# Optimization experiments

Hardware: AMD Instinct MI355X
Metric: run time of the kernel (lower is better)

The kernel has to match this reference:

```python
import jax, jax.numpy as jnp
import numpy as np

B, N, RD = 32, 2000, 32
E, H, A = 128, 256, 8
NUM_ACTIONS = N
ACTION_NORM = float(NUM_ACTIONS)


def _mlp2(x, W1, b1, W2, b2):
    return jnp.maximum(x @ W1 + b1, 0.0) @ W2 + b2


def setup_inputs() -> dict:
    key = jax.random.key(0)
    ks = jax.random.split(key, 8)
    s = lambda fan_in: 1.0 / np.sqrt(fan_in)
    return {
        "state": jax.random.normal(ks[0], (B, N, RD), jnp.float32),
        "distance_matrix": jax.random.uniform(ks[1], (N, N), jnp.float32),
        "W_emb1": jax.random.normal(ks[2], (RD, H), jnp.float32) * s(RD),
        "b_emb1": jnp.zeros((H,), jnp.float32),
        "W_emb2": jax.random.normal(ks[3], (H, E), jnp.float32) * s(H),
        "b_emb2": jnp.zeros((E,), jnp.float32),
        "Wq1": jax.random.normal(ks[4], (E + A, H), jnp.float32) * s(E + A),
        "bq1": jnp.zeros((H,), jnp.float32),
        "Wq2": jax.random.normal(ks[5], (H, 1), jnp.float32) * s(H),
        "bq2": jnp.zeros((1,), jnp.float32),
        "fixed_actions": jax.random.randint(ks[6], (3, B), 0, NUM_ACTIONS, jnp.int32),
        "fixed_agent_ids": jnp.arange(3, dtype=jnp.int32),
    }


def reference(state, distance_matrix, W_emb1, b_emb1, W_emb2, b_emb2,
              Wq1, bq1, Wq2, bq2, fixed_actions, fixed_agent_ids):
    # normalized distance -> similarity, row-stochastic
    dm = distance_matrix / distance_matrix.max()
    sim = jnp.exp(-dm)  # scaling = 1 (use_nn_scaling=False)
    sim = sim / sim.sum(-1, keepdims=True)

    enc = _mlp2(state, W_emb1, b_emb1, W_emb2, b_emb2)      # [B,N,E]
    x = jnp.einsum('nm,bme->bne', sim, enc)                 # graph conv mix

    idx_f = jnp.arange(N, dtype=x.dtype)

    def qnet(actions):
        # actions: [B,A] broadcast over node axis -> concat -> MLP -> [B,N]
        act = jnp.broadcast_to(actions[:, None, :], (B, N, A))
        feat = jnp.concatenate([x, act], axis=-1)           # [B,N,E+A]
        return _mlp2(feat, Wq1, bq1, Wq2, bq2)[..., 0]      # [B,N]

    # init actions: -1 everywhere, fixed agents get given action / norm
    actions = jnp.full((B, A), -1.0, dtype=x.dtype)
    actions = actions.at[:, fixed_agent_ids].set(
        fixed_actions.T.astype(x.dtype) / ACTION_NORM)

    # sequential per-agent soft-argmax loop (second torch loop; the first
    # torch loop's q-values are fully overwritten here, so it is dead code)
    q_cols = []
    for agent_id in range(A):
        q = qnet(actions)                                   # [B,N]
        sam = jnp.clip(jax.nn.softmax(q, axis=-1) @ idx_f, 0.0, float(NUM_ACTIONS))
        actions = actions.at[:, agent_id].set(
            jax.lax.stop_gradient(sam / ACTION_NORM))
        q2 = qnet(actions)
        qv = jnp.take_along_axis(q2, sam.astype(jnp.int32)[:, None], axis=-1)[:, 0]
        q_cols.append(qv)

    q_values = jnp.stack(q_cols, axis=1)                    # [B,A]
    chosen = (actions * ACTION_NORM).astype(jnp.int32)      # [B,A]
    return q_values, chosen
```

## Files before the change

### kernel.cpp

```cpp
#include <hip/hip_runtime.h>
#include <cstddef>

#define NB 32
#define NN 2000
#define NRD 32
#define NE 128
#define NH 256
#define NA 8
#define KP8 2048
#define NGP 128
#define H1S 264
#define XT8S 136
#define ACTION_NORM 2000.0f

typedef unsigned short u16;
typedef unsigned char u8;
typedef __bf16 b16x8 __attribute__((ext_vector_type(8)));
typedef float f32x4 __attribute__((ext_vector_type(4)));
typedef const __attribute__((address_space(1))) unsigned int* gptr_t;
typedef __attribute__((address_space(3))) unsigned int* lptr_t;

__device__ inline u16 f2bf(float x) {
    unsigned u = __float_as_uint(x);
    u += 0x7FFFu + ((u >> 16) & 1u);
    return (u16)(u >> 16);
}
__device__ inline float bf2f(u16 h) { return __uint_as_float((unsigned)h << 16); }
__device__ inline u8 f2fp8(float x) {
    return (u8)(__builtin_amdgcn_cvt_pk_fp8_f32(x, x, 0, false) & 0xFF);
}
__device__ inline u16 f2fp8x2(float a, float b) {
    return (u16)(__builtin_amdgcn_cvt_pk_fp8_f32(a, b, 0, false) & 0xFFFF);
}
__device__ inline float fp82f(u8 b) {
    return __builtin_amdgcn_cvt_pk_f32_fp8((unsigned)b, false)[0];
}
__device__ inline int kswz(int m) {
    return (m & ~63) + (((m >> 3) & 3) << 4) + (((m >> 5) & 1) << 3) + (m & 7);
}

#define PREP_STATE (64000 * 32)
#define PREP_W1T   (256 * 32)
#define PREP_W2T   (128 * 256)
#define PREP_WQ1T  (256 * 128)
#define PREP_PAD   (4096 * 48)
#define PREP_TOT   (PREP_STATE + PREP_W1T + PREP_W2T + PREP_WQ1T + PREP_PAD)
#define PREP_BLOCKS (PREP_TOT / 256)
#define MAX_BLOCKS 1024
__global__ __launch_bounds__(256) void k_front(
        const float* __restrict__ state, const float* __restrict__ W1,
        const float* __restrict__ W2, const float* __restrict__ Wq1,
        const float* __restrict__ dm, const int* __restrict__ fa,
        const int* __restrict__ fid,
        u16* __restrict__ state_b, u16* __restrict__ W1t,
        u16* __restrict__ W2t, u8* __restrict__ Wq1f8,
        u8* __restrict__ encb, float* __restrict__ pmax,
        float* __restrict__ actions, float* __restrict__ ap0,
        float2* __restrict__ part0) {
    __shared__ float sh[256];
    const int blk = blockIdx.x, t = threadIdx.x;
    if (blk < PREP_BLOCKS) {
        int i = blk * 256 + t;
        if (i < PREP_STATE) { state_b[i] = f2bf(state[i]); return; }
        i -= PREP_STATE;
        if (i < PREP_W1T) { int h = i >> 5, k = i & 31; W1t[i] = f2bf(W1[k * NH + h]); return; }
        i -= PREP_W1T;
        if (i < PREP_W2T) { int e = i >> 8, h = i & 255; W2t[i] = f2bf(W2[h * NE + e]); return; }
        i -= PREP_W2T;
        if (i < PREP_WQ1T) { int hq = i >> 7, e = i & 127; Wq1f8[i] = f2fp8(Wq1[e * NH + hq]); return; }
        i -= PREP_WQ1T;
        if (i < PREP_PAD) { int eb = i / 48, mm = NN + (i % 48); encb[(size_t)eb * KP8 + kswz(mm)] = 0; }
        return;
    }
    if (blk < PREP_BLOCKS + MAX_BLOCKS) {
        const int bid = blk - PREP_BLOCKS;
        float m = 0.0f;
        for (size_t i = (size_t)bid * 256 + t; i < (size_t)NN * NN; i += (size_t)MAX_BLOCKS * 256)
            m = fmaxf(m, dm[i]);
        sh[t] = m; __syncthreads();
        for (int s = 128; s > 0; s >>= 1) {
            if (t < s) sh[t] = fmaxf(sh[t], sh[t + s]);
            __syncthreads();
        }
        if (t == 0) pmax[bid] = sh[0];
        return;
    }
    const int b = t >> 3, a = t & 7;
    float v = -1.0f;
    for (int j = 0; j < 3; ++j)
        if (fid[j] == a) v = (float)fa[j * NB + b] / ACTION_NORM;
    actions[t] = v;
    sh[t] = v;
    __syncthreads();
    float wq[NA];
#pragma unroll
    for (int aa = 0; aa < NA; ++aa) wq[aa] = Wq1[(size_t)(NE + aa) * NH + t];
    for (int bb = 0; bb < NB; ++bb) {
        float s = 0.0f;
#pragma unroll
        for (int aa = 0; aa < NA; ++aa) s = fmaf(sh[bb * NA + aa], wq[aa], s);
        ap0[bb * NH + t] = s;
    }
    for (int i = t; i < NB * NGP; i += 256) part0[i] = make_float2(0.0f, 0.0f);
}

__global__ __launch_bounds__(512) void k_sim_enc(
        const u16* __restrict__ state_b, const u16* __restrict__ W1t,
        const u16* __restrict__ W2t, u8* __restrict__ encb,
        const float* __restrict__ b1, const float* __restrict__ b2,
        const float* __restrict__ dm, const float* __restrict__ pmax,
        u8* __restrict__ simb, float* __restrict__ inv_rs) {
    __shared__ u16 stage[20 * 512];
    __shared__ u16 h1t[64 * H1S];
    const int blk = blockIdx.x, tid = threadIdx.x;

    if (blk >= 1000) {
        float* shf = (float*)stage;
        const int n = blk - 1000, t = tid;
        float m = fmaxf(pmax[t], pmax[t + 512]);
        shf[t] = m; __syncthreads();
        for (int s = 256; s > 0; s >>= 1) {
            if (t < s) shf[t] = fmaxf(shf[t], shf[t + s]);
            __syncthreads();
        }
        const float inv = 1.0f / shf[0];
        __syncthreads();
        float s = 0.0f;
        for (int mm = t * 2; mm < KP8; mm += 1024) {
            float e0 = 0.0f, e1 = 0.0f;
            if (mm < NN)     { e0 = expf(-dm[(size_t)n * NN + mm] * inv);     s += e0; }
            if (mm + 1 < NN) { e1 = expf(-dm[(size_t)n * NN + mm + 1] * inv); s += e1; }
            *(u16*)(simb + (size_t)n * KP8 + kswz(mm)) = f2fp8x2(e0, e1);
        }
        shf[t] = s; __syncthreads();
        for (int st = 256; st > 0; st >>= 1) {
            if (t < st) shf[t] += shf[t + st];
            __syncthreads();
        }
        if (t == 0) inv_rs[n] = 1.0f / shf[0];
        return;
    }

    const int w = tid >> 6, l = tid & 63;
    const int lm = l & 15, lq = l >> 4;
    const int gm = blk * 64;

    {
#pragma unroll
        for (int i = 0; i < 3; ++i) {
            const int idx = w * 3 + i;
            if (idx < 20) {
                const u16* gp;
                if (idx < 4) gp = state_b + (size_t)(gm + idx * 16 + lm) * NRD + lq * 8;
                else         gp = W1t + (size_t)((idx - 4) * 16 + lm) * NRD + lq * 8;
                __builtin_amdgcn_global_load_lds((gptr_t)gp, (lptr_t)(stage + idx * 512), 16, 0, 0);
            }
        }
        __syncthreads();
        b16x8 af[4], bf[2];
#pragma unroll
        for (int i = 0; i < 4; ++i) af[i] = *(const b16x8*)(stage + i * 512 + l * 8);
#pragma unroll
        for (int j = 0; j < 2; ++j) bf[j] = *(const b16x8*)(stage + (4 + w * 2 + j) * 512 + l * 8);
        f32x4 acc1[4][2] = {};
#pragma unroll
        for (int i = 0; i < 4; ++i)
#pragma unroll
            for (int j = 0; j < 2; ++j)
                acc1[i][j] = __builtin_amdgcn_mfma_f32_16x16x32_bf16(af[i], bf[j], acc1[i][j], 0, 0, 0);
#pragma unroll
        for (int i = 0; i < 4; ++i)
#pragma unroll
            for (int r = 0; r < 4; ++r) {
                const int row = i * 16 + lq * 4 + r;
#pragma unroll
                for (int j = 0; j < 2; ++j) {
                    const int col = w * 32 + j * 16 + lm;
                    h1t[row * H1S + col] = f2bf(fmaxf(acc1[i][j][r] + b1[col], 0.0f));
                }
            }
    }

    const int wr = w & 3, wc = w >> 2;
    f32x4 acc2[2][2] = {};
    const u16* gpw = W2t + (size_t)(w * 16 + lm) * NH + lq * 8;
    __syncthreads();
    __builtin_amdgcn_global_load_lds((gptr_t)gpw, (lptr_t)(stage + w * 512), 16, 0, 0);
    __syncthreads();
    for (int t = 0; t < 8; ++t) {
        const int cur = t & 1;
        if (t < 7) {
            gpw += 32;
            __builtin_amdgcn_global_load_lds((gptr_t)gpw,
                (lptr_t)(stage + (cur ^ 1) * 4096 + w * 512), 16, 0, 0);
        }
        const u16* base = stage + cur * 4096;
        b16x8 af2[2], bf2[2];
#pragma unroll
        for (int i = 0; i < 2; ++i)
            af2[i] = *(const b16x8*)(base + (wr * 2 + i) * 512 + l * 8);
#pragma unroll
        for (int j = 0; j < 2; ++j)
            bf2[j] = *(const b16x8*)(h1t + (wc * 32 + j * 16 + lm) * H1S + t * 32 + lq * 8);
#pragma unroll
        for (int i = 0; i < 2; ++i)
#pragma unroll
            for (int j = 0; j < 2; ++j)
                acc2[i][j] = __builtin_amdgcn_mfma_f32_16x16x32_bf16(af2[i], bf2[j], acc2[i][j], 0, 0, 0);
        __syncthreads();
    }

    u8* etile = (u8*)stage;
#pragma unroll
    for (int i = 0; i < 2; ++i)
#pragma unroll
        for (int r = 0; r < 4; ++r) {
            const int e = wr * 32 + i * 16 + lq * 4 + r;
            const float bias = b2[e];
#pragma unroll
            for (int j = 0; j < 2; ++j) {
                const int off = wc * 32 + j * 16 + lm;
                etile[e * 64 + off] = f2fp8(acc2[i][j][r] + bias);
            }
        }
    __syncthreads();
#pragma unroll
    for (int u0 = 0; u0 < 2; ++u0) {
        const int u = u0 * 512 + tid;
        const int e = u >> 3, run = u & 7;
        const int rg0 = gm + run * 8;
        const unsigned bb = (unsigned)rg0 / 2000u;
        const unsigned m0 = (unsigned)rg0 - bb * 2000u;
        const int wbyte = (int)(m0 & ~63u) + (int)(((m0 >> 3) & 3u) << 4) + (int)(((m0 >> 5) & 1u) << 3);
        const uint2 v = *(const uint2*)(etile + e * 64 + run * 8);
        *(uint2*)(encb + ((size_t)bb * 128 + e) * KP8 + wbyte) = v;
    }
}

__global__ __launch_bounds__(512) void k_conv_y0(
        const u8* __restrict__ simb, const u8* __restrict__ encb,
        const u8* __restrict__ Wq1f8, const float* __restrict__ inv_rs,
        const float* __restrict__ bq1, const float* __restrict__ ap0,
        const float* __restrict__ Wq2, u8* __restrict__ y0f8,
        float2* __restrict__ part0) {
    __shared__ u8 lds[4 * 16384];
    __shared__ float qsum[64 * 8];
    const int tid = threadIdx.x;
    const int w = tid >> 6, l = tid & 63;
    const int wr = w & 1, wc = w >> 1;
    const int bm = blockIdx.x * 128;
    const int bb = blockIdx.y;
    const int lm = l & 15, lq = l >> 4;
    const u8* Bt = encb + (size_t)bb * 128 * KP8;
    typedef long lx2 __attribute__((ext_vector_type(2)));

    f32x4 acc[4][2] = {};

    const u8* gpt[2];
#pragma unroll
    for (int i = 0; i < 2; ++i) {
        const int idx = w * 2 + i;
        if (idx < 8) {
            int row = bm + idx * 16 + lm;
            row = row < NN ? row : NN - 1;
            gpt[i] = simb + (size_t)row * KP8 + lq * 16;
        } else {
            gpt[i] = Bt + (size_t)((idx - 8) * 16 + lm) * KP8 + lq * 16;
        }
    }

    auto STAGE = [&](int kt, int buf) {
#pragma unroll
        for (int i = 0; i < 2; ++i)
            __builtin_amdgcn_global_load_lds((gptr_t)(gpt[i] + kt * 64),
                (lptr_t)(lds + buf * 16384 + (w * 2 + i) * 1024), 16, 0, 0);
    };
    auto COMPUTE = [&](int buf) {
        const u8* curb = lds + buf * 16384;
        const int fo = l * 16;
        lx2 af[4], bf[2];
#pragma unroll
        for (int i = 0; i < 4; ++i)
            af[i] = *(const lx2*)(curb + (wr * 4 + i) * 1024 + fo);
#pragma unroll
        for (int j = 0; j < 2; ++j)
            bf[j] = *(const lx2*)(curb + (8 + wc * 2 + j) * 1024 + fo);
        __builtin_amdgcn_s_setprio(1);
#pragma unroll
        for (int i = 0; i < 4; ++i)
#pragma unroll
            for (int j = 0; j < 2; ++j) {
                acc[i][j] = __builtin_amdgcn_mfma_f32_16x16x32_fp8_fp8(af[i][0], bf[j][0], acc[i][j], 0, 0, 0);
                acc[i][j] = __builtin_amdgcn_mfma_f32_16x16x32_fp8_fp8(af[i][1], bf[j][1], acc[i][j], 0, 0, 0);
            }
        __builtin_amdgcn_s_setprio(0);
    };

#define FENCE() __builtin_amdgcn_sched_barrier(0)
#define BAR_VM(N) do { FENCE(); asm volatile("s_waitcnt vmcnt(" #N ")" ::: "memory"); \
    __builtin_amdgcn_s_barrier(); FENCE(); } while (0)

    STAGE(0, 0);
    STAGE(1, 1);
    for (int t = 0; t < 30; ++t) {
        STAGE(t + 2, (t + 2) & 3);
        BAR_VM(4);
        COMPUTE(t & 3);
    }
    BAR_VM(2);
    COMPUTE(2);
    BAR_VM(0);
    COMPUTE(3);
#undef BAR_VM
#undef FENCE

#pragma unroll
    for (int i = 0; i < 4; ++i) {
#pragma unroll
        for (int r = 0; r < 4; ++r) {
            const int row = wr * 64 + i * 16 + lq * 4 + r;
            const int gn = bm + row;
            const float rsv = inv_rs[gn < NN ? gn : NN - 1];
#pragma unroll
            for (int j = 0; j < 2; ++j) {
                const int col = wc * 32 + j * 16 + lm;
                lds[row * XT8S + col] = f2fp8(acc[i][j][r] * rsv);
            }
        }
    }
    __syncthreads();

    const int h0 = w * 32;
    float bq1v[2], apv[2], w2vv[2];
#pragma unroll
    for (int j = 0; j < 2; ++j) {
        const int h = h0 + j * 16 + lm;
        bq1v[j] = bq1[h];
        apv[j] = ap0[bb * NH + h];
        w2vv[j] = Wq2[h];
    }
    float se_tot = 0.0f, sn_tot = 0.0f;

    for (int half = 0; half < 2; ++half) {
        f32x4 acc2[4][2] = {};
#pragma unroll
        for (int ks = 0; ks < 4; ++ks) {
            long bfw[2];
#pragma unroll
            for (int j = 0; j < 2; ++j)
                bfw[j] = *(const long*)(Wq1f8 + (size_t)(h0 + j * 16 + lm) * NE + ks * 32 + lq * 8);
#pragma unroll
            for (int i = 0; i < 4; ++i) {
                const long afx = *(const long*)(lds + (half * 64 + i * 16 + lm) * XT8S + ks * 32 + lq * 8);
#pragma unroll
                for (int j = 0; j < 2; ++j)
                    acc2[i][j] = __builtin_amdgcn_mfma_f32_16x16x32_fp8_fp8(afx, bfw[j], acc2[i][j], 0, 0, 0);
            }
        }
#pragma unroll
        for (int i = 0; i < 4; ++i) {
#pragma unroll
            for (int r = 0; r < 4; ++r) {
                const int rl = i * 16 + lq * 4 + r;
                const int n = bm + half * 64 + rl;
                float q = 0.0f;
#pragma unroll
                for (int j = 0; j < 2; ++j) {
                    const float v = acc2[i][j][r] + bq1v[j];
                    if (n < NN) y0f8[((size_t)n * NB + bb) * NH + h0 + j * 16 + lm] = f2fp8(v);
                    q += fmaxf(v + apv[j], 0.0f) * w2vv[j];
                }
#pragma unroll
                for (int off = 1; off < 16; off <<= 1) q += __shfl_xor(q, off);
                if (lm == 0) qsum[rl * 8 + w] = q;
            }
        }
        __syncthreads();
        if (tid < 64) {
            const int n = bm + half * 64 + tid;
            float q = 0.0f;
#pragma unroll
            for (int wv = 0; wv < 8; ++wv) q += qsum[tid * 8 + wv];
            float e = (n < NN) ? expf(fminf(q, 60.0f)) : 0.0f;
            float sne = e * (float)n;
#pragma unroll
            for (int off = 32; off > 0; off >>= 1) {
                e += __shfl_xor(e, off); sne += __shfl_xor(sne, off);
            }
            if (tid == 0) { se_tot += e; sn_tot += sne; }
        }
        __syncthreads();
    }
    if (tid == 0) part0[bb * NGP + blockIdx.x] = make_float2(se_tot, sn_tot);
}

__global__ __launch_bounds__(256) void k_agent(
        const u8* __restrict__ y0f8, const float* __restrict__ Wq1,
        const float* __restrict__ Wq2, const float* __restrict__ bq2,
        float* actions, const float2* __restrict__ pin, float2* __restrict__ pout,
        float* __restrict__ out, int ag) {
    __shared__ float sh[256];
    __shared__ float s_sam;
    const int t = threadIdx.x;
    const int lane = t & 63, wave = t >> 6;
    const int wg = blockIdx.x * 4 + wave;
    const int b = wg & 31, ng = wg >> 5;
    const int hl = lane & 15, qtr = lane >> 4;

    float act[NA];
#pragma unroll
    for (int a = 0; a < NA; ++a) act[a] = actions[b * NA + a];
    {
        const float2 p0 = pin[b * NGP + lane];
        const float2 p1 = pin[b * NGP + 64 + lane];
        float se0 = p0.x + p1.x, sn0 = p0.y + p1.y;
#pragma unroll
        for (int m = 32; m > 0; m >>= 1) {
            se0 += __shfl_xor(se0, m); sn0 += __shfl_xor(sn0, m);
        }
        const float sam = fminf(fmaxf(sn0 / se0, 0.0f), 2000.0f);
        act[ag - 1] = sam * (1.0f / ACTION_NORM);
    }
    float ap16[16] = {};
#pragma unroll
    for (int a = 0; a < NA; ++a) {
        const float av = act[a];
        const float4* wq = (const float4*)(Wq1 + (size_t)(NE + a) * NH + hl * 16);
#pragma unroll
        for (int jj = 0; jj < 4; ++jj) {
            const float4 w4 = wq[jj];
            ap16[jj * 4 + 0] = fmaf(av, w4.x, ap16[jj * 4 + 0]);
            ap16[jj * 4 + 1] = fmaf(av, w4.y, ap16[jj * 4 + 1]);
            ap16[jj * 4 + 2] = fmaf(av, w4.z, ap16[jj * 4 + 2]);
            ap16[jj * 4 + 3] = fmaf(av, w4.w, ap16[jj * 4 + 3]);
        }
    }
    float w2v[16];
    {
        const float4* w2p = (const float4*)(Wq2 + hl * 16);
#pragma unroll
        for (int jj = 0; jj < 4; ++jj) {
            const float4 w4 = w2p[jj];
            w2v[jj * 4 + 0] = w4.x; w2v[jj * 4 + 1] = w4.y;
            w2v[jj * 4 + 2] = w4.z; w2v[jj * 4 + 3] = w4.w;
        }
    }

    float se = 0.0f, sn = 0.0f;
#pragma unroll
    for (int k = 0; k < 4; ++k) {
        const int p = ng + k * NGP;
        if (p >= NN / 4) break;
        const int n = 4 * p + qtr;
        const uint4 yv = *(const uint4*)(y0f8 + (((size_t)n * NB + b) << 8) + hl * 16);
        const unsigned dw[4] = {yv.x, yv.y, yv.z, yv.w};
        float q = 0.0f;
#pragma unroll
        for (int d = 0; d < 4; ++d) {
            const auto lo = __builtin_amdgcn_cvt_pk_f32_fp8(dw[d], false);
            const auto hi = __builtin_amdgcn_cvt_pk_f32_fp8(dw[d], true);
            q += fmaxf(lo[0] + ap16[d * 4 + 0], 0.f) * w2v[d * 4 + 0];
            q += fmaxf(lo[1] + ap16[d * 4 + 1], 0.f) * w2v[d * 4 + 1];
            q += fmaxf(hi[0] + ap16[d * 4 + 2], 0.f) * w2v[d * 4 + 2];
            q += fmaxf(hi[1] + ap16[d * 4 + 3], 0.f) * w2v[d * 4 + 3];
        }
#pragma unroll
        for (int off = 1; off < 16; off <<= 1) q += __shfl_xor(q, off);
        const float e = expf(fminf(q, 60.0f));
        se += e; sn += e * (float)n;
    }
    se += __shfl_xor(se, 16); sn += __shfl_xor(sn, 16);
    se += __shfl_xor(se, 32); sn += __shfl_xor(sn, 32);
    if (lane == 0) pout[b * NGP + ng] = make_float2(se, sn);

    if (blockIdx.x < NB) {
        const int bb = blockIdx.x;
        if (wave == 0) {
            const float2 p0 = pin[bb * NGP + lane];
            const float2 p1 = pin[bb * NGP + 64 + lane];
            float a1 = p0.x + p1.x, a2 = p0.y + p1.y;
#pragma unroll
            for (int m = 32; m > 0; m >>= 1) {
                a1 += __shfl_xor(a1, m); a2 += __shfl_xor(a2, m);
            }
            if (lane == 0) s_sam = fminf(fmaxf(a2 / a1, 0.0f), 2000.0f);
        }
        __syncthreads();
        const float sam = s_sam;
        const float samn = sam * (1.0f / ACTION_NORM);
        float apt = 0.0f;
#pragma unroll
        for (int a = 0; a < NA; ++a) {
            const float av = (a == ag - 1) ? samn : actions[bb * NA + a];
            apt = fmaf(av, Wq1[(size_t)(NE + a) * NH + t], apt);
        }
        int nsel = (int)sam; if (nsel > NN - 1) nsel = NN - 1;
        const float yv = fp82f(y0f8[((size_t)nsel * NB + bb) * NH + t]);
        sh[t] = fmaxf(yv + apt, 0.0f) * Wq2[t];
        __syncthreads();
        for (int s = 128; s > 0; s >>= 1) {
            if (t < s) sh[t] += sh[t + s];
            __syncthreads();
        }
        if (t == 0) {
            out[bb * NA + (ag - 1)] = sh[0] + bq2[0];
            actions[bb * NA + (ag - 1)] = samn;
        }
    }
}

__global__ __launch_bounds__(256) void k_fin(
        const u8* __restrict__ y0f8, const float* __restrict__ Wq1,
        const float* __restrict__ Wq2, const float* __restrict__ bq2,
        const float* __restrict__ actions, const float2* __restrict__ pin,
        float* __restrict__ out) {
    __shared__ float sh[256];
    __shared__ float s_sam;
    const int bb = blockIdx.x, t = threadIdx.x;
    const int lane = t & 63, wave = t >> 6;
    if (wave == 0) {
        const float2 p0 = pin[bb * NGP + lane];
        const float2 p1 = pin[bb * NGP + 64 + lane];
        float a1 = p0.x + p1.x, a2 = p0.y + p1.y;
#pragma unroll
        for (int m = 32; m > 0; m >>= 1) {
            a1 += __shfl_xor(a1, m); a2 += __shfl_xor(a2, m);
        }
        if (lane == 0) s_sam = fminf(fmaxf(a2 / a1, 0.0f), 2000.0f);
    }
    __syncthreads();
    const float sam = s_sam;
    const float samn = sam * (1.0f / ACTION_NORM);
    float apt = 0.0f;
#pragma unroll
    for (int a = 0; a < NA; ++a) {
        const float av = (a == NA - 1) ? samn : actions[bb * NA + a];
        apt = fmaf(av, Wq1[(size_t)(NE + a) * NH + t], apt);
    }
    int nsel = (int)sam; if (nsel > NN - 1) nsel = NN - 1;
    const float yv = fp82f(y0f8[((size_t)nsel * NB + bb) * NH + t]);
    sh[t] = fmaxf(yv + apt, 0.0f) * Wq2[t];
    __syncthreads();
    for (int s = 128; s > 0; s >>= 1) {
        if (t < s) sh[t] += sh[t + s];
        __syncthreads();
    }
    if (t == 0) out[bb * NA + (NA - 1)] = sh[0] + bq2[0];
    if (t < NA) {
        const float av = (t == NA - 1) ? samn : actions[bb * NA + t];
        out[NB * NA + bb * NA + t] = (float)(int)(av * ACTION_NORM);
    }
}

extern "C" void kernel_launch(void* const* d_in, const int* in_sizes, int n_in,
                              void* d_out, int out_size, void* d_ws, size_t ws_size,
                              hipStream_t stream) {
    const float* state = (const float*)d_in[0];
    const float* dm    = (const float*)d_in[1];
    const float* W1    = (const float*)d_in[2];
    const float* b1    = (const float*)d_in[3];
    const float* W2    = (const float*)d_in[4];
    const float* b2    = (const float*)d_in[5];
    const float* Wq1   = (const float*)d_in[6];
    const float* bq1   = (const float*)d_in[7];
    const float* Wq2   = (const float*)d_in[8];
    const float* bq2   = (const float*)d_in[9];
    const int* fa      = (const int*)d_in[10];
    const int* fid     = (const int*)d_in[11];
    float* out = (float*)d_out;

    char* p = (char*)d_ws;
    u8* simb       = (u8*)p;       p += (size_t)NN * KP8;
    u8* encb       = (u8*)p;       p += (size_t)4096 * KP8;
    float* inv_rs  = (float*)p;    p += 2048 * 4;
    float* pmax    = (float*)p;    p += 1024 * 4;
    float* actions = (float*)p;    p += 256 * 4;
    float* ap0     = (float*)p;    p += 8192 * 4;
    float2* part0  = (float2*)p;   p += (size_t)NB * NGP * 8;
    float2* part1  = (float2*)p;   p += (size_t)NB * NGP * 8;
    u16* state_b   = (u16*)p;      p += (size_t)2048000 * 2;
    u16* W1t       = (u16*)p;      p += 8192 * 2;
    u16* W2t       = (u16*)p;      p += 32768 * 2;
    u8* Wq1f8      = (u8*)p;       p += 32768;
    u8* y0f8       = (u8*)p;       p += (size_t)16384000;

    k_front<<<PREP_BLOCKS + MAX_BLOCKS + 1, 256, 0, stream>>>(
        state, W1, W2, Wq1, dm, fa, fid,
        state_b, W1t, W2t, Wq1f8, encb, pmax, actions, ap0, part0);
    k_sim_enc<<<3000, 512, 0, stream>>>(state_b, W1t, W2t, encb, b1, b2,
                                        dm, pmax, simb, inv_rs);
    k_conv_y0<<<dim3(16, 32), 512, 0, stream>>>(simb, encb, Wq1f8, inv_rs, bq1,
                                                ap0, Wq2, y0f8, part0);
    for (int ag = 1; ag < NA; ++ag) {
        const float2* pin  = (ag & 1) ? part0 : part1;
        float2*       pout = (ag & 1) ? part1 : part0;
        k_agent<<<1024, 256, 0, stream>>>(y0f8, Wq1, Wq2, bq2, actions,
                                          pin, pout, out, ag);
    }
    k_fin<<<NB, 256, 0, stream>>>(y0f8, Wq1, Wq2, bq2, actions, part1, out);
}
```

Before: 256.8 us.

## Split sim/enc kernels, incremental action projection, and hoisted y0 loads in agent

```diff
diff --git a/kernel.cpp b/kernel.cpp
--- a/kernel.cpp
+++ b/kernel.cpp
@@ -104,43 +104,43 @@
     for (int i = t; i < NB * NGP; i += 256) part0[i] = make_float2(0.0f, 0.0f);
 }
 
-__global__ __launch_bounds__(512) void k_sim_enc(
+__global__ __launch_bounds__(512) void k_sim(
+        const float* __restrict__ dm, const float* __restrict__ pmax,
+        u8* __restrict__ simb, float* __restrict__ inv_rs) {
+    __shared__ float shf[512];
+    __shared__ u8 srow[KP8];
+    const int n = blockIdx.x, t = threadIdx.x;
+    float m = fmaxf(pmax[t], pmax[t + 512]);
+    shf[t] = m; __syncthreads();
+    for (int s = 256; s > 0; s >>= 1) {
+        if (t < s) shf[t] = fmaxf(shf[t], shf[t + s]);
+        __syncthreads();
+    }
+    const float inv = 1.0f / shf[0];
+    __syncthreads();
+    float s = 0.0f;
+    for (int mm = t * 2; mm < KP8; mm += 1024) {
+        float e0 = 0.0f, e1 = 0.0f;
+        if (mm < NN)     { e0 = expf(-dm[(size_t)n * NN + mm] * inv);     s += e0; }
+        if (mm + 1 < NN) { e1 = expf(-dm[(size_t)n * NN + mm + 1] * inv); s += e1; }
+        *(u16*)(srow + kswz(mm)) = f2fp8x2(e0, e1);
+    }
+    shf[t] = s; __syncthreads();
+    for (int st = 256; st > 0; st >>= 1) {
+        if (t < st) shf[t] += shf[t + st];
+        __syncthreads();
+    }
+    if (t == 0) inv_rs[n] = 1.0f / shf[0];
+    if (t < 128) *(uint4*)(simb + (size_t)n * KP8 + t * 16) = *(const uint4*)(srow + t * 16);
+}
+
+__global__ __launch_bounds__(512) void k_enc(
         const u16* __restrict__ state_b, const u16* __restrict__ W1t,
         const u16* __restrict__ W2t, u8* __restrict__ encb,
-        const float* __restrict__ b1, const float* __restrict__ b2,
-        const float* __restrict__ dm, const float* __restrict__ pmax,
-        u8* __restrict__ simb, float* __restrict__ inv_rs) {
+        const float* __restrict__ b1, const float* __restrict__ b2) {
     __shared__ u16 stage[20 * 512];
     __shared__ u16 h1t[64 * H1S];
     const int blk = blockIdx.x, tid = threadIdx.x;
-
-    if (blk >= 1000) {
-        float* shf = (float*)stage;
-        const int n = blk - 1000, t = tid;
-        float m = fmaxf(pmax[t], pmax[t + 512]);
-        shf[t] = m; __syncthreads();
-        for (int s = 256; s > 0; s >>= 1) {
-            if (t < s) shf[t] = fmaxf(shf[t], shf[t + s]);
-            __syncthreads();
-        }
-        const float inv = 1.0f / shf[0];
-        __syncthreads();
-        float s = 0.0f;
-        for (int mm = t * 2; mm < KP8; mm += 1024) {
-            float e0 = 0.0f, e1 = 0.0f;
-            if (mm < NN)     { e0 = expf(-dm[(size_t)n * NN + mm] * inv);     s += e0; }
-            if (mm + 1 < NN) { e1 = expf(-dm[(size_t)n * NN + mm + 1] * inv); s += e1; }
-            *(u16*)(simb + (size_t)n * KP8 + kswz(mm)) = f2fp8x2(e0, e1);
-        }
-        shf[t] = s; __syncthreads();
-        for (int st = 256; st > 0; st >>= 1) {
-            if (t < st) shf[t] += shf[t + st];
-            __syncthreads();
-        }
-        if (t == 0) inv_rs[n] = 1.0f / shf[0];
-        return;
-    }
-
     const int w = tid >> 6, l = tid & 63;
     const int lm = l & 15, lq = l >> 4;
     const int gm = blk * 64;
@@ -397,7 +397,9 @@
 __global__ __launch_bounds__(256) void k_agent(
         const u8* __restrict__ y0f8, const float* __restrict__ Wq1,
         const float* __restrict__ Wq2, const float* __restrict__ bq2,
-        float* actions, const float2* __restrict__ pin, float2* __restrict__ pout,
+        float* actions, const int* __restrict__ fa, const int* __restrict__ fid,
+        const float* __restrict__ apb, float* __restrict__ apbase_out,
+        const float2* __restrict__ pin, float2* __restrict__ pout,
         float* __restrict__ out, int ag) {
     __shared__ float sh[256];
     __shared__ float s_sam;
@@ -406,10 +408,9 @@
     const int wg = blockIdx.x * 4 + wave;
     const int b = wg & 31, ng = wg >> 5;
     const int hl = lane & 15, qtr = lane >> 4;
-
-    float act[NA];
-#pragma unroll
-    for (int a = 0; a < NA; ++a) act[a] = actions[b * NA + a];
+    const int idx = ag - 1;
+
+    float samn;
     {
         const float2 p0 = pin[b * NGP + lane];
         const float2 p1 = pin[b * NGP + 64 + lane];
@@ -419,55 +420,57 @@
             se0 += __shfl_xor(se0, m); sn0 += __shfl_xor(sn0, m);
         }
         const float sam = fminf(fmaxf(sn0 / se0, 0.0f), 2000.0f);
-        act[ag - 1] = sam * (1.0f / ACTION_NORM);
-    }
-    float ap16[16] = {};
-#pragma unroll
-    for (int a = 0; a < NA; ++a) {
-        const float av = act[a];
-        const float4* wq = (const float4*)(Wq1 + (size_t)(NE + a) * NH + hl * 16);
+        samn = sam * (1.0f / ACTION_NORM);
+    }
+    float iv = -1.0f;
+    for (int j = 0; j < 3; ++j)
+        if (fid[j] == idx) iv = (float)fa[j * NB + b] * (1.0f / ACTION_NORM);
+    const float d = samn - iv;
+
+    float ap16[16], w2v[16];
+    {
+        const float4* ab  = (const float4*)(apb + b * NH + hl * 16);
+        const float4* wq  = (const float4*)(Wq1 + (size_t)(NE + idx) * NH + hl * 16);
+        const float4* w2p = (const float4*)(Wq2 + hl * 16);
 #pragma unroll
         for (int jj = 0; jj < 4; ++jj) {
-            const float4 w4 = wq[jj];
-            ap16[jj * 4 + 0] = fmaf(av, w4.x, ap16[jj * 4 + 0]);
-            ap16[jj * 4 + 1] = fmaf(av, w4.y, ap16[jj * 4 + 1]);
-            ap16[jj * 4 + 2] = fmaf(av, w4.z, ap16[jj * 4 + 2]);
-            ap16[jj * 4 + 3] = fmaf(av, w4.w, ap16[jj * 4 + 3]);
-        }
-    }
-    float w2v[16];
-    {
-        const float4* w2p = (const float4*)(Wq2 + hl * 16);
-#pragma unroll
-        for (int jj = 0; jj < 4; ++jj) {
-            const float4 w4 = w2p[jj];
-            w2v[jj * 4 + 0] = w4.x; w2v[jj * 4 + 1] = w4.y;
-            w2v[jj * 4 + 2] = w4.z; w2v[jj * 4 + 3] = w4.w;
-        }
-    }
-
+            const float4 a4 = ab[jj]; const float4 w4 = wq[jj]; const float4 v4 = w2p[jj];
+            ap16[jj * 4 + 0] = fmaf(d, w4.x, a4.x);
+            ap16[jj * 4 + 1] = fmaf(d, w4.y, a4.y);
+            ap16[jj * 4 + 2] = fmaf(d, w4.z, a4.z);
+            ap16[jj * 4 + 3] = fmaf(d, w4.w, a4.w);
+            w2v[jj * 4 + 0] = v4.x; w2v[jj * 4 + 1] = v4.y;
+            w2v[jj * 4 + 2] = v4.z; w2v[jj * 4 + 3] = v4.w;
+        }
+    }
+
+    uint4 yv[4];
+#pragma unroll
+    for (int k = 0; k < 4; ++k) {
+        const int n = 4 * (ng + k * NGP) + qtr;
+        yv[k] = *(const uint4*)(y0f8 + (((size_t)n * NB + b) << 8) + hl * 16);
+    }
     float se = 0.0f, sn = 0.0f;
 #pragma unroll
     for (int k = 0; k < 4; ++k) {
-        const int p = ng + k * NGP;
-        if (p >= NN / 4) break;
-        const int n = 4 * p + qtr;
-        const uint4 yv = *(const uint4*)(y0f8 + (((size_t)n * NB + b) << 8) + hl * 16);
-        const unsigned dw[4] = {yv.x, yv.y, yv.z, yv.w};
+        const int n = 4 * (ng + k * NGP) + qtr;
+        const unsigned dw[4] = {yv[k].x, yv[k].y, yv[k].z, yv[k].w};
         float q = 0.0f;
 #pragma unroll
-        for (int d = 0; d < 4; ++d) {
-            const auto lo = __builtin_amdgcn_cvt_pk_f32_fp8(dw[d], false);
-            const auto hi = __builtin_amdgcn_cvt_pk_f32_fp8(dw[d], true);
-            q += fmaxf(lo[0] + ap16[d * 4 + 0], 0.f) * w2v[d * 4 + 0];
-            q += fmaxf(lo[1] + ap16[d * 4 + 1], 0.f) * w2v[d * 4 + 1];
-            q += fmaxf(hi[0] + ap16[d * 4 + 2], 0.f) * w2v[d * 4 + 2];
-            q += fmaxf(hi[1] + ap16[d * 4 + 3], 0.f) * w2v[d * 4 + 3];
+        for (int dd = 0; dd < 4; ++dd) {
+            const auto lo = __builtin_amdgcn_cvt_pk_f32_fp8(dw[dd], false);
+            const auto hi = __builtin_amdgcn_cvt_pk_f32_fp8(dw[dd], true);
+            q += fmaxf(lo[0] + ap16[dd * 4 + 0], 0.f) * w2v[dd * 4 + 0];
+            q += fmaxf(lo[1] + ap16[dd * 4 + 1], 0.f) * w2v[dd * 4 + 1];
+            q += fmaxf(hi[0] + ap16[dd * 4 + 2], 0.f) * w2v[dd * 4 + 2];
+            q += fmaxf(hi[1] + ap16[dd * 4 + 3], 0.f) * w2v[dd * 4 + 3];
         }
 #pragma unroll
         for (int off = 1; off < 16; off <<= 1) q += __shfl_xor(q, off);
-        const float e = expf(fminf(q, 60.0f));
-        se += e; sn += e * (float)n;
+        if (n < NN) {
+            const float e = expf(fminf(q, 60.0f));
+            se += e; sn += e * (float)n;
+        }
     }
     se += __shfl_xor(se, 16); sn += __shfl_xor(sn, 16);
     se += __shfl_xor(se, 32); sn += __shfl_xor(sn, 32);
@@ -487,24 +490,25 @@
         }
         __syncthreads();
         const float sam = s_sam;
-        const float samn = sam * (1.0f / ACTION_NORM);
+        const float samf = sam * (1.0f / ACTION_NORM);
         float apt = 0.0f;
 #pragma unroll
         for (int a = 0; a < NA; ++a) {
-            const float av = (a == ag - 1) ? samn : actions[bb * NA + a];
+            const float av = (a == idx) ? samf : actions[bb * NA + a];
             apt = fmaf(av, Wq1[(size_t)(NE + a) * NH + t], apt);
         }
+        apbase_out[bb * NH + t] = apt;
         int nsel = (int)sam; if (nsel > NN - 1) nsel = NN - 1;
-        const float yv = fp82f(y0f8[((size_t)nsel * NB + bb) * NH + t]);
-        sh[t] = fmaxf(yv + apt, 0.0f) * Wq2[t];
+        const float yv2 = fp82f(y0f8[((size_t)nsel * NB + bb) * NH + t]);
+        sh[t] = fmaxf(yv2 + apt, 0.0f) * Wq2[t];
         __syncthreads();
         for (int s = 128; s > 0; s >>= 1) {
             if (t < s) sh[t] += sh[t + s];
             __syncthreads();
         }
         if (t == 0) {
-            out[bb * NA + (ag - 1)] = sh[0] + bq2[0];
-            actions[bb * NA + (ag - 1)] = samn;
+            out[bb * NA + idx] = sh[0] + bq2[0];
+            actions[bb * NA + idx] = samf;
         }
     }
 }
@@ -576,25 +580,30 @@
     float* pmax    = (float*)p;    p += 1024 * 4;
     float* actions = (float*)p;    p += 256 * 4;
     float* ap0     = (float*)p;    p += 8192 * 4;
+    float* apbA    = (float*)p;    p += 8192 * 4;
+    float* apbB    = (float*)p;    p += 8192 * 4;
     float2* part0  = (float2*)p;   p += (size_t)NB * NGP * 8;
     float2* part1  = (float2*)p;   p += (size_t)NB * NGP * 8;
     u16* state_b   = (u16*)p;      p += (size_t)2048000 * 2;
     u16* W1t       = (u16*)p;      p += 8192 * 2;
     u16* W2t       = (u16*)p;      p += 32768 * 2;
     u8* Wq1f8      = (u8*)p;       p += 32768;
-    u8* y0f8       = (u8*)p;       p += (size_t)16384000;
+    u8* y0f8       = (u8*)p;       p += (size_t)2048 * NB * NH;
 
     k_front<<<PREP_BLOCKS + MAX_BLOCKS + 1, 256, 0, stream>>>(
         state, W1, W2, Wq1, dm, fa, fid,
         state_b, W1t, W2t, Wq1f8, encb, pmax, actions, ap0, part0);
-    k_sim_enc<<<3000, 512, 0, stream>>>(state_b, W1t, W2t, encb, b1, b2,
-                                        dm, pmax, simb, inv_rs);
+    k_sim<<<NN, 512, 0, stream>>>(dm, pmax, simb, inv_rs);
+    k_enc<<<1000, 512, 0, stream>>>(state_b, W1t, W2t, encb, b1, b2);
     k_conv_y0<<<dim3(16, 32), 512, 0, stream>>>(simb, encb, Wq1f8, inv_rs, bq1,
                                                 ap0, Wq2, y0f8, part0);
     for (int ag = 1; ag < NA; ++ag) {
         const float2* pin  = (ag & 1) ? part0 : part1;
         float2*       pout = (ag & 1) ? part1 : part0;
+        const float*  apb  = (ag == 1) ? ap0 : ((ag & 1) ? apbB : apbA);
+        float*        apo  = (ag & 1) ? apbA : apbB;
         k_agent<<<1024, 256, 0, stream>>>(y0f8, Wq1, Wq2, bq2, actions,
+                                          fa, fid, apb, apo,
                                           pin, pout, out, ag);
     }
     k_fin<<<NB, 256, 0, stream>>>(y0f8, Wq1, Wq2, bq2, actions, part1, out);
```

Measured after the change: 226.0 us. 1.14x faster.
